# Optimization experiments

Hardware: AMD Instinct MI355X
Metric: run time of the kernel (lower is better)

Reference implementation:

```python
import jax, jax.numpy as jnp
import numpy as np

NUM_EXPERTS = 4  # matches init_kwargs

def setup_inputs() -> dict:
    key = jax.random.key(0)
    ks = jax.random.split(key, 6)
    B, T, D = 4, 4096, 1024
    H = 4 * D
    x = jax.random.normal(ks[0], (B, T, D), dtype=jnp.float32)
    token_mask = jax.random.randint(ks[1], (B, T), 0, NUM_EXPERTS, dtype=jnp.int32)
    s1 = 1.0 / np.sqrt(D)
    s2 = 1.0 / np.sqrt(H)
    W1 = jax.random.normal(ks[2], (H, D), dtype=jnp.float32) * s1
    b1 = jax.random.normal(ks[3], (H,), dtype=jnp.float32) * s1
    W2 = jax.random.normal(ks[4], (D, H), dtype=jnp.float32) * s2
    b2 = jax.random.normal(ks[5], (D,), dtype=jnp.float32) * s2
    return {"x": x, "token_mask": token_mask, "W1": W1, "b1": b1, "W2": W2, "b2": b2}

def reference(x, token_mask, W1, b1, W2, b2):
    # Nested MoE FFN: expert m uses leading D//2^(E-1-m) input dims and
    # leading H//2^(E-1-m) hidden dims; top expert (m=E-1) is the full MLP.
    D = x.shape[-1]
    H = W1.shape[0]
    factor = 2 ** (NUM_EXPERTS - 1 - token_mask)          # [B,T] int
    d_in = D // factor                                     # [B,T]
    d_hid = H // factor                                    # [B,T]
    mask_in = (jnp.arange(D) < d_in[..., None]).astype(x.dtype)    # [B,T,D]
    mask_hid = (jnp.arange(H) < d_hid[..., None]).astype(x.dtype)  # [B,T,H]
    # Expand: slice input dims, project, keep only nested hidden slice (bias included only there)
    h = (jnp.einsum('btd,hd->bth', x * mask_in, W1) + b1) * mask_hid
    h = jax.nn.gelu(h, approximate=False)  # gelu(0)=0 preserves nested zeros
    # Contract: zeros outside the nested hidden slice contribute nothing; full output + bias
    out = jnp.einsum('bth,dh->btd', h, W2) + b2
    return out
```

## Files before the change

kernel.cpp:

```cpp
#include <hip/hip_runtime.h>
#include <cstdint>
#include <math.h>

typedef __attribute__((ext_vector_type(8))) __bf16 bf16x8;
typedef __attribute__((ext_vector_type(4))) float f32x4;
typedef unsigned short ushort_t;

__device__ __forceinline__ ushort_t f2bf(float f) {
    uint32_t u = __float_as_uint(f);
    u += 0x7fff + ((u >> 16) & 1);
    return (ushort_t)(u >> 16);
}

__device__ __forceinline__ float gelu_exact(float v) {
    return 0.5f * v * (1.0f + erff(v * 0.70710678118654752440f));
}

__global__ void convert_w2_kernel(const float* __restrict__ s1, const float* __restrict__ s2,
                                  ushort_t* __restrict__ d1, ushort_t* __restrict__ d2,
                                  int n4) {
    int i = blockIdx.x * blockDim.x + threadIdx.x;
    const float* src; ushort_t* dst; int k;
    if (i < n4) { src = s1; dst = d1; k = i; }
    else if (i < 2 * n4) { src = s2; dst = d2; k = i - n4; }
    else return;
    const float4 v = ((const float4*)src)[k];
    ushort4 o;
    o.x = f2bf(v.x); o.y = f2bf(v.y); o.z = f2bf(v.z); o.w = f2bf(v.w);
    ((ushort4*)dst)[k] = o;
}

#define SORT_T 256
__global__ void sort_kernel(const int* __restrict__ tm, int M, int D, int H,
                            int* __restrict__ meta, int* __restrict__ sidx) {
    __shared__ int lc[4][SORT_T + 1];
    __shared__ int soff[4];
    const int t = threadIdx.x;
    const int nj = M / SORT_T;
    int c0 = 0, c1 = 0, c2 = 0, c3 = 0;
    for (int j = 0; j < nj; j++) {
        int e = tm[t + j * SORT_T];
        c0 += (e == 0); c1 += (e == 1); c2 += (e == 2); c3 += (e == 3);
    }
    lc[0][t + 1] = c0; lc[1][t + 1] = c1; lc[2][t + 1] = c2; lc[3][t + 1] = c3;
    if (t < 4) lc[t][0] = 0;
    __syncthreads();
    if (t < 4) {
        int acc = 0;
        for (int i = 1; i <= SORT_T; i++) { acc += lc[t][i]; lc[t][i] = acc; }
    }
    __syncthreads();
    if (t == 0) {
        int off = 0, xoff = 0, hoff = 0;
        for (int e = 0; e < 4; e++) {
            int c = lc[e][SORT_T];
            int ac = (c + 127) & ~127;
            int din = D >> (3 - e), dh = H >> (3 - e);
            meta[e] = c; meta[4 + e] = off; meta[8 + e] = ac; meta[12 + e] = ac >> 7;
            meta[16 + e] = xoff; meta[20 + e] = hoff;
            soff[e] = off;
            off += ac; xoff += ac * din; hoff += ac * dh;
        }
        meta[28] = off;
        int a = 0, b = 0;
        for (int k = 0; k < 4; k++) {
            int e = 3 - k;
            meta[24 + k] = a; a += meta[12 + e] * ((H >> (3 - e)) >> 7);
            meta[32 + k] = b; b += meta[12 + e] * (D >> 7);
        }
        meta[29] = a; meta[36] = b;
    }
    __syncthreads();
    int pos[4];
    pos[0] = soff[0] + lc[0][t]; pos[1] = soff[1] + lc[1][t];
    pos[2] = soff[2] + lc[2][t]; pos[3] = soff[3] + lc[3][t];
    for (int j = 0; j < nj; j++) {
        int i = t + j * SORT_T;
        int e = tm[i];
        sidx[pos[e]++] = i;
    }
    __syncthreads();
    for (int e = 0; e < 4; e++) {
        int s = soff[e] + lc[e][SORT_T];
        int n = meta[8 + e] - lc[e][SORT_T];
        for (int i = t; i < n; i += SORT_T) sidx[s + i] = -1;
    }
}

__global__ void convert_x_sorted(const float* __restrict__ x,
                                 const int* __restrict__ meta,
                                 const int* __restrict__ sidx,
                                 ushort_t* __restrict__ xb, int D) {
    const int p = blockIdx.x;
    if (p >= meta[28]) return;
    const int e = (p >= meta[5]) + (p >= meta[6]) + (p >= meta[7]);
    const int off = meta[4 + e];
    const int din = D >> (3 - e);
    const int tok = sidx[p];
    ushort_t* dst = xb + (size_t)meta[16 + e] + (size_t)(p - off) * din;
    if (tok < 0) {
        for (int c = threadIdx.x * 4; c < din; c += blockDim.x * 4)
            *(ushort4*)(dst + c) = ushort4{0, 0, 0, 0};
    } else {
        const float* src = x + (size_t)tok * D;
        for (int c = threadIdx.x * 4; c < din; c += blockDim.x * 4) {
            const float4 v = *(const float4*)(src + c);
            ushort4 o;
            o.x = f2bf(v.x); o.y = f2bf(v.y); o.z = f2bf(v.z); o.w = f2bf(v.w);
            *(ushort4*)(dst + c) = o;
        }
    }
}

template <int EPI>
__global__ void gemm_sorted(const ushort_t* __restrict__ Abuf,
                            const ushort_t* __restrict__ Bw,
                            const float* __restrict__ bias,
                            const int* __restrict__ meta,
                            const int* __restrict__ sidx,
                            ushort_t* __restrict__ hb,
                            float* __restrict__ out,
                            int D, int H) {
    __shared__ ushort_t As[128 * 32];
    __shared__ ushort_t Bs[128 * 32];

    const int t    = threadIdx.x;
    const int wave = t >> 6;
    const int lane = t & 63;
    const int quad = lane >> 4;
    const int l16  = lane & 15;
    const int wm   = wave & 1;
    const int wn   = wave >> 1;
    const int srow = t >> 2;
    const int scol = (t & 3) * 8;
    char* AsB = (char*)As;
    char* BsB = (char*)Bs;
    const int ldsoff = wave * 64 * 16;

    const int* st = meta + (EPI == 0 ? 24 : 32);
    const int  T  = meta[EPI == 0 ? 29 : 36];

    for (int idx = blockIdx.x; idx < T; idx += gridDim.x) {
        const int k3 = (idx >= st[1]) + (idx >= st[2]) + (idx >= st[3]);
        const int e = 3 - k3;
        const int local = idx - st[k3];
        const int mtiles = meta[12 + e];
        const int mt = local % mtiles;
        const int nt = local / mtiles;

        const int K   = (EPI == 0) ? (D >> (3 - e)) : (H >> (3 - e));
        const int Ne  = (EPI == 0) ? (H >> (3 - e)) : D;
        const int lda = K;
        const int ldb = (EPI == 0) ? D : H;
        const int nb  = nt * 128;
        const ushort_t* A = Abuf + (size_t)((EPI == 0) ? meta[16 + e] : meta[20 + e]);

        const ushort_t* Ag = A + (size_t)(mt * 128 + srow) * lda + scol;
        const ushort_t* Bg = Bw + (size_t)(nb + srow) * ldb + scol;

        f32x4 acc[4][4] = {};

        for (int kt = 0; kt < K; kt += 32) {
            __syncthreads();
            __builtin_amdgcn_global_load_lds(
                (__attribute__((address_space(1))) void*)(uintptr_t)(Ag + kt),
                (__attribute__((address_space(3))) void*)(AsB + ldsoff), 16, 0, 0);
            __builtin_amdgcn_global_load_lds(
                (__attribute__((address_space(1))) void*)(uintptr_t)(Ag + (size_t)64 * lda + kt),
                (__attribute__((address_space(3))) void*)(AsB + 4096 + ldsoff), 16, 0, 0);
            __builtin_amdgcn_global_load_lds(
                (__attribute__((address_space(1))) void*)(uintptr_t)(Bg + kt),
                (__attribute__((address_space(3))) void*)(BsB + ldsoff), 16, 0, 0);
            __builtin_amdgcn_global_load_lds(
                (__attribute__((address_space(1))) void*)(uintptr_t)(Bg + (size_t)64 * ldb + kt),
                (__attribute__((address_space(3))) void*)(BsB + 4096 + ldsoff), 16, 0, 0);
            __syncthreads();

            bf16x8 af[4], bfr[4];
#pragma unroll
            for (int i = 0; i < 4; i++) {
                af[i]  = *(const bf16x8*)(As + (wm * 64 + i * 16 + l16) * 32 + quad * 8);
                bfr[i] = *(const bf16x8*)(Bs + (wn * 64 + i * 16 + l16) * 32 + quad * 8);
            }
#pragma unroll
            for (int i = 0; i < 4; i++)
#pragma unroll
                for (int j = 0; j < 4; j++)
                    acc[i][j] = __builtin_amdgcn_mfma_f32_16x16x32_bf16(af[i], bfr[j], acc[i][j], 0, 0, 0);
        }

        const int colbase = nb + wn * 64 + l16;
        float bv[4];
#pragma unroll
        for (int j = 0; j < 4; j++) bv[j] = bias[colbase + j * 16];

#pragma unroll
        for (int i = 0; i < 4; i++) {
#pragma unroll
            for (int r = 0; r < 4; r++) {
                const int lrow = mt * 128 + wm * 64 + i * 16 + quad * 4 + r;
                if (EPI == 0) {
                    ushort_t* dst = hb + (size_t)meta[20 + e] + (size_t)lrow * Ne;
#pragma unroll
                    for (int j = 0; j < 4; j++)
                        dst[colbase + j * 16] = f2bf(gelu_exact(acc[i][j][r] + bv[j]));
                } else {
                    const int tok = sidx[meta[4 + e] + lrow];
                    if (tok >= 0) {
                        float* dst = out + (size_t)tok * D;
#pragma unroll
                        for (int j = 0; j < 4; j++)
                            dst[colbase + j * 16] = acc[i][j][r] + bv[j];
                    }
                }
            }
        }
    }
}

__global__ void naive_kernel(const float* __restrict__ x, const int* __restrict__ tm,
                             const float* __restrict__ W1, const float* __restrict__ b1,
                             const float* __restrict__ W2, const float* __restrict__ b2,
                             float* __restrict__ out, int D, int Hdim) {
    const int t = blockIdx.x;
    const int m = tm[t];
    const int din = D >> (3 - m);
    const int dh = Hdim >> (3 - m);
    extern __shared__ float sm[];
    float* xs = sm;
    float* hs = sm + D;
    for (int i = threadIdx.x; i < din; i += blockDim.x) xs[i] = x[(size_t)t * D + i];
    __syncthreads();
    for (int h = threadIdx.x; h < dh; h += blockDim.x) {
        const float* w = W1 + (size_t)h * D;
        float a = b1[h];
        for (int d = 0; d < din; d++) a += xs[d] * w[d];
        hs[h] = gelu_exact(a);
    }
    __syncthreads();
    for (int d = threadIdx.x; d < D; d += blockDim.x) {
        const float* w = W2 + (size_t)d * Hdim;
        float a = b2[d];
        for (int h = 0; h < dh; h++) a += hs[h] * w[h];
        out[(size_t)t * D + d] = a;
    }
}

extern "C" void kernel_launch(void* const* d_in, const int* in_sizes, int n_in,
                              void* d_out, int out_size, void* d_ws, size_t ws_size,
                              hipStream_t stream) {
    const float* x  = (const float*)d_in[0];
    const int* tm   = (const int*)d_in[1];
    const float* W1 = (const float*)d_in[2];
    const float* b1 = (const float*)d_in[3];
    const float* W2 = (const float*)d_in[4];
    const float* b2 = (const float*)d_in[5];
    float* out = (float*)d_out;

    const int M    = in_sizes[1];
    const int Hdim = in_sizes[3];
    const int D    = in_sizes[0] / M;

    const int Mpad = M + 512;
    const size_t meta_sz = 256;
    const size_t sidx_sz = ((size_t)Mpad * 4 + 255) & ~(size_t)255;
    const size_t xb_sz   = (size_t)Mpad * D * 2;
    const size_t w1_sz   = (size_t)Hdim * D * 2;
    const size_t w2_sz   = (size_t)D * Hdim * 2;
    const size_t hb_sz   = (size_t)Mpad * Hdim * 2;
    const size_t need_sorted = meta_sz + sidx_sz + xb_sz + w1_sz + w2_sz + hb_sz;

    const bool shape_ok = (M % 256 == 0) && (D % 128 == 0) && (Hdim % 128 == 0) &&
                          (D >= 1024) && (Hdim >= 4096);

    if (shape_ok && ws_size >= need_sorted) {
        char* p = (char*)d_ws;
        int* meta     = (int*)p;        p += meta_sz;
        int* sidx     = (int*)p;        p += sidx_sz;
        ushort_t* xb  = (ushort_t*)p;   p += xb_sz;
        ushort_t* w1b = (ushort_t*)p;   p += w1_sz;
        ushort_t* w2b = (ushort_t*)p;   p += w2_sz;
        ushort_t* hb  = (ushort_t*)p;

        sort_kernel<<<1, SORT_T, 0, stream>>>(tm, M, D, Hdim, meta, sidx);
        const int n4w = Hdim * D / 4;
        convert_w2_kernel<<<(2 * n4w + 255) / 256, 256, 0, stream>>>(W1, W2, w1b, w2b, n4w);
        convert_x_sorted<<<Mpad, 64, 0, stream>>>(x, meta, sidx, xb, D);

        gemm_sorted<0><<<2048, 256, 0, stream>>>(xb, w1b, b1, meta, sidx, hb, nullptr, D, Hdim);
        gemm_sorted<1><<<2048, 256, 0, stream>>>(hb, w2b, b2, meta, sidx, nullptr, out, D, Hdim);
        return;
    }

    const size_t shmem = (size_t)(D + Hdim) * sizeof(float);
    naive_kernel<<<M, 256, shmem, stream>>>(x, tm, W1, b1, W2, b2, out, D, Hdim);
}
```

Before: 373.1 us.

## Add split-K for large experts in second GEMM and atomic tile queue

The second GEMM now splits the K dimension for experts with hidden size above 1024. Partial sums go to an fp32 buffer, and a new reduce kernel adds them together with the bias. Both GEMMs now take work tiles from an atomic counter instead of a fixed grid stride, so the largest experts' tiles start first and load balances better. The cost is extra memory traffic for the partial buffer, an additional kernel launch, and an atomic plus a barrier per tile.

```diff
diff --git a/kernel.cpp b/kernel.cpp
--- a/kernel.cpp
+++ b/kernel.cpp
@@ -32,7 +32,7 @@
 
 #define SORT_T 256
 __global__ void sort_kernel(const int* __restrict__ tm, int M, int D, int H,
-                            int* __restrict__ meta, int* __restrict__ sidx) {
+                            int* __restrict__ meta, int* __restrict__ sidx, int splitk) {
     __shared__ int lc[4][SORT_T + 1];
     __shared__ int soff[4];
     const int t = threadIdx.x;
@@ -65,10 +65,19 @@
         int a = 0, b = 0;
         for (int k = 0; k < 4; k++) {
             int e = 3 - k;
-            meta[24 + k] = a; a += meta[12 + e] * ((H >> (3 - e)) >> 7);
-            meta[32 + k] = b; b += meta[12 + e] * (D >> 7);
+            int Ke = H >> (3 - e);
+            int s = (splitk && Ke > 1024) ? (Ke >> 10) : 1;
+            meta[48 + e] = s;
+            meta[24 + k] = a; a += meta[12 + e] * (Ke >> 7);
+            meta[32 + k] = b; b += meta[12 + e] * (D >> 7) * s;
         }
         meta[29] = a; meta[36] = b;
+        int poff = 0;
+        for (int e = 0; e < 4; e++) {
+            meta[44 + e] = poff;
+            if (meta[48 + e] > 1) poff += meta[8 + e] * D * meta[48 + e];
+        }
+        meta[40] = 0; meta[41] = 0;
     }
     __syncthreads();
     int pos[4];
@@ -120,9 +129,12 @@
                             const int* __restrict__ sidx,
                             ushort_t* __restrict__ hb,
                             float* __restrict__ out,
+                            float* __restrict__ pbuf,
+                            int* __restrict__ qc,
                             int D, int H) {
     __shared__ ushort_t As[128 * 32];
     __shared__ ushort_t Bs[128 * 32];
+    __shared__ int s_idx;
 
     const int t    = threadIdx.x;
     const int wave = t >> 6;
@@ -140,27 +152,42 @@
     const int* st = meta + (EPI == 0 ? 24 : 32);
     const int  T  = meta[EPI == 0 ? 29 : 36];
 
-    for (int idx = blockIdx.x; idx < T; idx += gridDim.x) {
+    for (;;) {
+        if (t == 0) s_idx = atomicAdd(qc, 1);
+        __syncthreads();
+        const int idx = s_idx;
+        if (idx >= T) break;
+
         const int k3 = (idx >= st[1]) + (idx >= st[2]) + (idx >= st[3]);
         const int e = 3 - k3;
         const int local = idx - st[k3];
         const int mtiles = meta[12 + e];
-        const int mt = local % mtiles;
-        const int nt = local / mtiles;
-
-        const int K   = (EPI == 0) ? (D >> (3 - e)) : (H >> (3 - e));
+        const int Kfull = (EPI == 0) ? (D >> (3 - e)) : (H >> (3 - e));
+        int mt, nt, sk = 0, s = 1;
+        if (EPI == 0) {
+            mt = local % mtiles;
+            nt = local / mtiles;
+        } else {
+            s = meta[48 + e];
+            mt = local % mtiles;
+            const int q = local / mtiles;
+            sk = q - (q / s) * s;
+            nt = q / s;
+        }
+        const int Kc = Kfull / s;
+        const int kbeg = sk * Kc;
         const int Ne  = (EPI == 0) ? (H >> (3 - e)) : D;
-        const int lda = K;
+        const int lda = Kfull;
         const int ldb = (EPI == 0) ? D : H;
         const int nb  = nt * 128;
         const ushort_t* A = Abuf + (size_t)((EPI == 0) ? meta[16 + e] : meta[20 + e]);
 
-        const ushort_t* Ag = A + (size_t)(mt * 128 + srow) * lda + scol;
-        const ushort_t* Bg = Bw + (size_t)(nb + srow) * ldb + scol;
+        const ushort_t* Ag = A + (size_t)(mt * 128 + srow) * lda + kbeg + scol;
+        const ushort_t* Bg = Bw + (size_t)(nb + srow) * ldb + kbeg + scol;
 
         f32x4 acc[4][4] = {};
 
-        for (int kt = 0; kt < K; kt += 32) {
+        for (int kt = 0; kt < Kc; kt += 32) {
             __syncthreads();
             __builtin_amdgcn_global_load_lds(
                 (__attribute__((address_space(1))) void*)(uintptr_t)(Ag + kt),
@@ -190,21 +217,31 @@
         }
 
         const int colbase = nb + wn * 64 + l16;
-        float bv[4];
-#pragma unroll
-        for (int j = 0; j < 4; j++) bv[j] = bias[colbase + j * 16];
-
-#pragma unroll
-        for (int i = 0; i < 4; i++) {
-#pragma unroll
-            for (int r = 0; r < 4; r++) {
-                const int lrow = mt * 128 + wm * 64 + i * 16 + quad * 4 + r;
-                if (EPI == 0) {
+
+        if (EPI == 0) {
+            float bv[4];
+#pragma unroll
+            for (int j = 0; j < 4; j++) bv[j] = bias[colbase + j * 16];
+#pragma unroll
+            for (int i = 0; i < 4; i++) {
+#pragma unroll
+                for (int r = 0; r < 4; r++) {
+                    const int lrow = mt * 128 + wm * 64 + i * 16 + quad * 4 + r;
                     ushort_t* dst = hb + (size_t)meta[20 + e] + (size_t)lrow * Ne;
 #pragma unroll
                     for (int j = 0; j < 4; j++)
                         dst[colbase + j * 16] = f2bf(gelu_exact(acc[i][j][r] + bv[j]));
-                } else {
+                }
+            }
+        } else if (s == 1) {
+            float bv[4];
+#pragma unroll
+            for (int j = 0; j < 4; j++) bv[j] = bias[colbase + j * 16];
+#pragma unroll
+            for (int i = 0; i < 4; i++) {
+#pragma unroll
+                for (int r = 0; r < 4; r++) {
+                    const int lrow = mt * 128 + wm * 64 + i * 16 + quad * 4 + r;
                     const int tok = sidx[meta[4 + e] + lrow];
                     if (tok >= 0) {
                         float* dst = out + (size_t)tok * D;
@@ -214,7 +251,45 @@
                     }
                 }
             }
-        }
+        } else {
+            float* pb = pbuf + meta[44 + e] + (size_t)sk * meta[8 + e] * D;
+#pragma unroll
+            for (int i = 0; i < 4; i++) {
+#pragma unroll
+                for (int r = 0; r < 4; r++) {
+                    const int lrow = mt * 128 + wm * 64 + i * 16 + quad * 4 + r;
+                    float* dst = pb + (size_t)lrow * D;
+#pragma unroll
+                    for (int j = 0; j < 4; j++)
+                        dst[colbase + j * 16] = acc[i][j][r];
+                }
+            }
+        }
+        __syncthreads();
+    }
+}
+
+__global__ void reduce_out(const float* __restrict__ pbuf, const float* __restrict__ b2,
+                           const int* __restrict__ meta, const int* __restrict__ sidx,
+                           float* __restrict__ out, int D) {
+    const int p = blockIdx.x;
+    if (p >= meta[28]) return;
+    const int e = (p >= meta[5]) + (p >= meta[6]) + (p >= meta[7]);
+    const int s = meta[48 + e];
+    if (s == 1) return;
+    const int tok = sidx[p];
+    if (tok < 0) return;
+    const int lrow = p - meta[4 + e];
+    const float* src = pbuf + meta[44 + e] + (size_t)lrow * D;
+    const size_t stride = (size_t)meta[8 + e] * D;
+    float* dst = out + (size_t)tok * D;
+    for (int c = threadIdx.x * 4; c < D; c += blockDim.x * 4) {
+        float4 a = *(const float4*)(b2 + c);
+        for (int k = 0; k < s; k++) {
+            const float4 v = *(const float4*)(src + k * stride + c);
+            a.x += v.x; a.y += v.y; a.z += v.z; a.w += v.w;
+        }
+        *(float4*)(dst + c) = a;
     }
 }
 
@@ -270,25 +345,35 @@
     const size_t hb_sz   = (size_t)Mpad * Hdim * 2;
     const size_t need_sorted = meta_sz + sidx_sz + xb_sz + w1_sz + w2_sz + hb_sz;
 
+    const int s3 = (Hdim > 1024) ? (Hdim / 1024) : 1;
+    const size_t pbuf_sz = (size_t)Mpad * D * s3 * 4;
+    const size_t need_split = need_sorted + pbuf_sz;
+
     const bool shape_ok = (M % 256 == 0) && (D % 128 == 0) && (Hdim % 128 == 0) &&
                           (D >= 1024) && (Hdim >= 4096);
 
     if (shape_ok && ws_size >= need_sorted) {
+        const int splitk = (ws_size >= need_split) ? 1 : 0;
         char* p = (char*)d_ws;
         int* meta     = (int*)p;        p += meta_sz;
         int* sidx     = (int*)p;        p += sidx_sz;
         ushort_t* xb  = (ushort_t*)p;   p += xb_sz;
         ushort_t* w1b = (ushort_t*)p;   p += w1_sz;
         ushort_t* w2b = (ushort_t*)p;   p += w2_sz;
-        ushort_t* hb  = (ushort_t*)p;
-
-        sort_kernel<<<1, SORT_T, 0, stream>>>(tm, M, D, Hdim, meta, sidx);
+        ushort_t* hb  = (ushort_t*)p;   p += hb_sz;
+        float* pbuf   = (float*)p;
+
+        sort_kernel<<<1, SORT_T, 0, stream>>>(tm, M, D, Hdim, meta, sidx, splitk);
         const int n4w = Hdim * D / 4;
         convert_w2_kernel<<<(2 * n4w + 255) / 256, 256, 0, stream>>>(W1, W2, w1b, w2b, n4w);
         convert_x_sorted<<<Mpad, 64, 0, stream>>>(x, meta, sidx, xb, D);
 
-        gemm_sorted<0><<<2048, 256, 0, stream>>>(xb, w1b, b1, meta, sidx, hb, nullptr, D, Hdim);
-        gemm_sorted<1><<<2048, 256, 0, stream>>>(hb, w2b, b2, meta, sidx, nullptr, out, D, Hdim);
+        gemm_sorted<0><<<2048, 256, 0, stream>>>(xb, w1b, b1, meta, sidx, hb, nullptr,
+                                                 pbuf, meta + 40, D, Hdim);
+        gemm_sorted<1><<<2048, 256, 0, stream>>>(hb, w2b, b2, meta, sidx, nullptr, out,
+                                                 pbuf, meta + 41, D, Hdim);
+        if (splitk)
+            reduce_out<<<Mpad, 256, 0, stream>>>(pbuf, b2, meta, sidx, out, D);
         return;
     }
 
```

Result: slower. 401.2 us (+7.5%).
